# Performance work log

Measured on AMD Instinct MI355X. Metric: run time of the kernel, lower is better.

The kernel has to match this reference:

```python
import jax, jax.numpy as jnp
import numpy as np

PAD = 0  # pad_token_id sentinel used for word_starts and labels_arcs masking


def setup_inputs() -> dict:
    B, S, H, L = 16, 256, 768, 37
    key = jax.random.key(0)
    k1, k2, k3, k4, k5 = jax.random.split(key, 5)
    hidden = jax.random.normal(k1, (B, S, H), dtype=jnp.float32)
    # strictly-increasing subword start indices (1,3,5,...), zero-padded to S
    n_starts = S // 2
    row = jnp.concatenate([
        1 + 2 * jnp.arange(n_starts, dtype=jnp.int32),
        jnp.zeros(S - n_starts, dtype=jnp.int32),
    ])
    word_starts = jnp.tile(row[None, :], (B, 1))
    n_words = n_starts - 1  # spans are between consecutive starts
    la = jax.random.randint(k2, (B, S), 1, 2 * S, dtype=jnp.int32)
    labels_arcs = jnp.where(jnp.arange(S)[None, :] < n_words, la, PAD)
    labels_rels = jax.random.randint(k3, (B, S), 0, L, dtype=jnp.int32)
    W_arc = jax.random.normal(k4, (H + 1, H), dtype=jnp.float32) * 0.02
    W_rel = jax.random.normal(k5, (L, H + 1, H + 1), dtype=jnp.float32) * 0.02
    return dict(hidden=hidden, W_arc=W_arc, W_rel=W_rel,
                word_starts=word_starts, labels_arcs=labels_arcs,
                labels_rels=labels_rels)


def _merge_subword_tokens(hidden, word_starts):
    """Fused segment-mean: word j = mean(hidden[start_j:start_{j+1}])."""
    B, S, H = hidden.shape
    csum = jnp.concatenate(
        [jnp.zeros((B, 1, H), hidden.dtype), jnp.cumsum(hidden, axis=1)], axis=1)
    n_valid = jnp.sum(word_starts != PAD, axis=1)  # [B]
    start = word_starts  # [B,S]
    end = jnp.concatenate(
        [word_starts[:, 1:], jnp.zeros((B, 1), word_starts.dtype)], axis=1)
    valid = (jnp.arange(S)[None, :] + 1) < n_valid[:, None]  # word j needs start j+1
    s0 = jnp.take_along_axis(csum, start[..., None].astype(jnp.int32), axis=1)
    s1 = jnp.take_along_axis(csum, end[..., None].astype(jnp.int32), axis=1)
    length = jnp.clip(end - start, 1, None).astype(hidden.dtype)[..., None]
    return jnp.where(valid[..., None], (s1 - s0) / length, 0.0)  # [B,S,H]


def _with_ones(x):
    return jnp.concatenate([x, jnp.ones_like(x[..., :1])], axis=-1)


def reference(hidden, W_arc, W_rel, word_starts, labels_arcs, labels_rels):
    deps = _merge_subword_tokens(hidden, word_starts)            # [B,S,H]
    heads = jnp.concatenate([hidden, deps], axis=1)              # [B,2S,H]
    xa = _with_ones(deps)                                        # [B,S,H+1]
    arc_preds = jnp.einsum('bxi,ij,byj->bxy', xa, W_arc, heads)  # [B,S,2S]
    yr = _with_ones(heads)                                       # [B,2S,H+1]
    rel_preds = jnp.einsum('bxi,oij,byj->bxyo', xa, W_rel, yr)   # [B,S,2S,L]

    B, S, Y, L = rel_preds.shape
    mask = (labels_arcs != PAD).astype(hidden.dtype)             # [B,S]
    n = jnp.sum(mask)
    arc_lp = jax.nn.log_softmax(arc_preds, axis=-1)
    safe_arcs = jnp.clip(labels_arcs, 0, Y - 1)
    arc_ll = jnp.take_along_axis(arc_lp, safe_arcs[..., None], axis=-1)[..., 0]
    arc_loss = -jnp.sum(arc_ll * mask) / n

    idx = jnp.broadcast_to(safe_arcs[:, :, None, None], (B, S, 1, L))
    rel_sel = jnp.take_along_axis(rel_preds, idx, axis=2)[:, :, 0, :]  # [B,S,L]
    rel_lp = jax.nn.log_softmax(rel_sel, axis=-1)
    rel_ll = jnp.take_along_axis(rel_lp, labels_rels[..., None], axis=-1)[..., 0]
    rel_loss = -jnp.sum(rel_ll * mask) / n

    loss = arc_loss + rel_loss
    return loss, rel_preds, arc_preds
```

## Files before the change

### kernel.cpp

```cpp
#include <hip/hip_runtime.h>
#include <cmath>
#include <cstdint>


#define NB 16
#define SS 256
#define HH 768
#define LLn 37
#define YY 512

static const long long REL_ELEMS = (long long)NB * SS * YY * LLn;

typedef __bf16 bf16_t;
typedef __bf16 bf16x8 __attribute__((ext_vector_type(8)));
typedef float f32x4 __attribute__((ext_vector_type(4)));

__device__ __forceinline__ void async_copy16(const void* g, void* l) {
  __builtin_amdgcn_global_load_lds((__attribute__((address_space(1))) void*)(g),
                                   (__attribute__((address_space(3))) void*)(l),
                                   16, 0, 0);
}

__device__ __forceinline__ float wave_max(float v) {
  #pragma unroll
  for (int off = 32; off > 0; off >>= 1) v = fmaxf(v, __shfl_xor(v, off));
  return v;
}
__device__ __forceinline__ float wave_sum(float v) {
  #pragma unroll
  for (int off = 32; off > 0; off >>= 1) v += __shfl_xor(v, off);
  return v;
}


__global__ void hid_rows(const float* __restrict__ hidden, bf16_t* __restrict__ yrb) {
  const long long r = blockIdx.x;
  const int b = (int)(r >> 8), y = (int)(r & 255);
  const float4* src = (const float4*)(hidden + r * HH);
  bf16_t* dst = yrb + ((long long)b * YY + y) * HH;
  const int t = threadIdx.x;
  const float4 v = src[t];
  bf16_t o4[4] = {(bf16_t)v.x, (bf16_t)v.y, (bf16_t)v.z, (bf16_t)v.w};
  *(ushort4*)(dst + t * 4) = *(ushort4*)o4;
}

__global__ void build_deps2(const float* __restrict__ hidden,
                            const int* __restrict__ word_starts,
                            bf16_t* __restrict__ yrb) {
  const int x = blockIdx.x, b = blockIdx.y, t = threadIdx.x;
  const int ws0 = word_starts[b * SS + x];
  const int ws1 = (x + 1 < SS) ? word_starts[b * SS + x + 1] : 0;
  const bool valid = (x + 1 < SS) && (ws1 != 0);
  const int start = min(max(ws0, 0), SS);
  const int end = min(max(ws1, 0), SS);
  const int len = max(end - start, 1);
  const float inv = 1.0f / (float)len;
  const float* hb = hidden + (long long)b * SS * HH;
  bf16_t* yr = yrb + ((long long)b * YY + SS + x) * HH;
  for (int h = t; h < HH; h += 256) {
    float s = 0.f;
    if (valid) for (int tt = start; tt < end; ++tt) s += hb[(long long)tt * HH + h];
    yr[h] = (bf16_t)(valid ? s * inv : 0.f);
  }
}

__global__ void conv_warc(const float* __restrict__ W, bf16_t* __restrict__ Wab) {
  __shared__ float tbuf[32][33];
  const int i0 = blockIdx.x * 32, j0 = blockIdx.y * 32;
  const int tx = threadIdx.x, ty = threadIdx.y;
  for (int rr = 0; rr < 32; rr += 8)
    tbuf[ty + rr][tx] = W[(long long)(i0 + ty + rr) * HH + j0 + tx];
  __syncthreads();
  for (int rr = 0; rr < 32; rr += 8)
    Wab[(long long)(j0 + ty + rr) * HH + i0 + tx] = (bf16_t)tbuf[tx][ty + rr];
}

__global__ void conv_wrel(const float* __restrict__ W, bf16_t* __restrict__ Wb, int o0) {
  __shared__ float tbuf[32][33];
  const int o = o0 + blockIdx.z;
  const int i0 = blockIdx.x * 32, j0 = blockIdx.y * 32;
  const int tx = threadIdx.x, ty = threadIdx.y;
  const float* Wo = W + (long long)o * (HH + 1) * (HH + 1);
  for (int rr = 0; rr < 32; rr += 8)
    tbuf[ty + rr][tx] = Wo[(long long)(i0 + ty + rr) * (HH + 1) + j0 + tx];
  __syncthreads();
  bf16_t* Wbo = Wb + (long long)blockIdx.z * HH * HH;
  for (int rr = 0; rr < 32; rr += 8)
    Wbo[(long long)(j0 + ty + rr) * HH + i0 + tx] = (bf16_t)tbuf[tx][ty + rr];
}

__global__ void build_misc(const float* __restrict__ W_rel, const float* __restrict__ W_arc,
                           float* __restrict__ WbiasJ, bf16_t* __restrict__ Wb768,
                           float* __restrict__ bias768b, float* __restrict__ biasArc,
                           float* __restrict__ lossacc) {
  const int blk = blockIdx.x, t = threadIdx.x;
  if (blk < LLn) {
    const int o = blk;
    const float* Wo = W_rel + (long long)o * (HH + 1) * (HH + 1);
    for (int j = t; j < HH; j += 256)
      WbiasJ[(long long)o * HH + j] = Wo[(long long)HH * (HH + 1) + j];
    for (int i = t; i < HH; i += 256)
      Wb768[(long long)o * HH + i] = (bf16_t)Wo[(long long)i * (HH + 1) + HH];
    if (t == 0) bias768b[o] = Wo[(long long)HH * (HH + 1) + HH];
  } else {
    for (int j = t; j < HH; j += 256) biasArc[j] = W_arc[(long long)HH * HH + j];
    if (t == 0) { lossacc[0] = 0.f; lossacc[1] = 0.f; }
  }
}

__global__ void bias2_kernel(const bf16_t* __restrict__ yrb,
                             const bf16_t* __restrict__ Wb768,
                             const float* __restrict__ bias768b,
                             float* __restrict__ d_bias2) {
  const int r = blockIdx.x;
  const int b = r >> 8, x = r & 255;
  const bf16_t* dep = yrb + ((long long)b * YY + SS + x) * HH;
  const int w = threadIdx.x >> 6, lane = threadIdx.x & 63;
  __shared__ float drow[HH];
  for (int h = threadIdx.x; h < HH; h += 256) drow[h] = (float)dep[h];
  __syncthreads();
  for (int o = w; o < LLn; o += 4) {
    const bf16_t* wrow = Wb768 + (long long)o * HH;
    float s = 0.f;
    #pragma unroll
    for (int i = 0; i < HH / 64; i++) s += drow[lane + 64 * i] * (float)wrow[lane + 64 * i];
    s = wave_sum(s);
    if (lane == 0) d_bias2[(long long)r * 128 + o] = s + bias768b[o];
  }
}


template<int MODE>
__global__ __launch_bounds__(256)
void gemm_bt(const bf16_t* __restrict__ A, long long sAz, int lda, int aview,
             const bf16_t* __restrict__ B, long long sBz, int ldb,
             int K,
             float* __restrict__ Cf, bf16_t* __restrict__ Cb,
             long long sCz, int ldc,
             const float* __restrict__ cbias, int sbias,
             int OC, int o0, const float* __restrict__ bias_xo,
             int gy, int gx) {
  __shared__ __align__(16) char smem_raw[32768];
  bf16_t* const lds = (bf16_t*)smem_raw;
  const int tid = threadIdx.x;
  const int w = tid >> 6;
  const int lane = tid & 63;

  const int nwg = (int)gridDim.x;
  const int q = nwg >> 3, r8 = nwg & 7;
  const int xcd = (int)blockIdx.x & 7, sub = (int)blockIdx.x >> 3;
  const int lid = ((xcd < r8) ? xcd * (q + 1) : r8 * (q + 1) + (xcd - r8) * q) + sub;
  const int yb = lid % gy;
  const int t2g = lid / gy;
  const int xb = t2g % gx;
  const int z = t2g / gx;

  const long long row0 = (long long)yb * 128;
  const long long col0 = (long long)xb * 128;
  const bf16_t* Ab;
  if (aview) {
    const long long bb = row0 >> 8;
    Ab = A + (bb * 512 + 256 + (row0 & 255)) * (long long)lda;
  } else {
    Ab = A + z * sAz + row0 * lda;
  }
  const bf16_t* Bb = B + z * sBz + col0 * ldb;

  const int r_in = lane >> 2;
  const int kofs = (lane & 3) * 8;
  const bf16_t* gA0 = Ab + (long long)(w * 32 + r_in) * lda + kofs;
  const bf16_t* gA1 = gA0 + 16ll * lda;
  const bf16_t* gB0 = Bb + (long long)(w * 32 + r_in) * ldb + kofs;
  const bf16_t* gB1 = gB0 + 16ll * ldb;
  const int lA0 = (w * 32) * 32;
  const int lA1 = (w * 32 + 16) * 32;
  const int lB0 = 4096 + (w * 32) * 32;
  const int lB1 = 4096 + (w * 32 + 16) * 32;

  f32x4 acc[4][4];
  #pragma unroll
  for (int i = 0; i < 4; i++)
    #pragma unroll
    for (int j = 0; j < 4; j++)
      #pragma unroll
      for (int e = 0; e < 4; e++) acc[i][j][e] = 0.f;

  const int wm = (w >> 1) * 64, wn = (w & 1) * 64;
  const int fr = lane & 15;
  const int fq = lane >> 4;
  const int aoff = fq * 8;

  async_copy16(gA0, lds + lA0);
  async_copy16(gA1, lds + lA1);
  async_copy16(gB0, lds + lB0);
  async_copy16(gB1, lds + lB1);
  __syncthreads();

  int cur = 0;
  for (int k0 = 32; k0 < K; k0 += 32) {
    bf16_t* nb = lds + (cur ^ 1) * 8192;
    async_copy16(gA0 + k0, nb + lA0);
    async_copy16(gA1 + k0, nb + lA1);
    async_copy16(gB0 + k0, nb + lB0);
    async_copy16(gB1 + k0, nb + lB1);
    const bf16_t* cb = lds + cur * 8192;
    bf16x8 af[4], bfr[4];
    #pragma unroll
    for (int t = 0; t < 4; t++) af[t]  = *(const bf16x8*)&cb[(wm + t * 16 + fr) * 32 + aoff];
    #pragma unroll
    for (int t = 0; t < 4; t++) bfr[t] = *(const bf16x8*)&cb[4096 + (wn + t * 16 + fr) * 32 + aoff];
    #pragma unroll
    for (int tm = 0; tm < 4; tm++)
      #pragma unroll
      for (int tn = 0; tn < 4; tn++)
        acc[tm][tn] = __builtin_amdgcn_mfma_f32_16x16x32_bf16(af[tm], bfr[tn], acc[tm][tn], 0, 0, 0);
    __syncthreads();
    cur ^= 1;
  }
  {
    const bf16_t* cb = lds + cur * 8192;
    bf16x8 af[4], bfr[4];
    #pragma unroll
    for (int t = 0; t < 4; t++) af[t]  = *(const bf16x8*)&cb[(wm + t * 16 + fr) * 32 + aoff];
    #pragma unroll
    for (int t = 0; t < 4; t++) bfr[t] = *(const bf16x8*)&cb[4096 + (wn + t * 16 + fr) * 32 + aoff];
    #pragma unroll
    for (int tm = 0; tm < 4; tm++)
      #pragma unroll
      for (int tn = 0; tn < 4; tn++)
        acc[tm][tn] = __builtin_amdgcn_mfma_f32_16x16x32_bf16(af[tm], bfr[tn], acc[tm][tn], 0, 0, 0);
  }

  if (MODE == 2) {
    __syncthreads();
    float* ebuf = (float*)smem_raw;
    const int c = tid & 127;
    const int rgrp = tid >> 7;
    const int n = (int)col0 + c;
    const int x = n / OC;
    const int o = o0 + (n - x * OC);
    const float bias = bias_xo[(((long long)z << 8) + x) * 128 + o];
    float* outp = Cf + z * sCz + (long long)x * (YY * LLn) + o;
    #pragma unroll
    for (int ch = 0; ch < 4; ch++) {
      #pragma unroll
      for (int tn = 0; tn < 4; tn++)
        #pragma unroll
        for (int e = 0; e < 4; e++)
          ebuf[((w >> 1) * 16 + fq * 4 + e) * 132 + wn + tn * 16 + fr] = acc[ch][tn][e];
      __syncthreads();
      const long long ybase = row0 + (long long)rgrp * 64 + ch * 16;
      #pragma unroll
      for (int r = 0; r < 16; r++)
        outp[(ybase + r) * LLn] = ebuf[(rgrp * 16 + r) * 132 + c] + bias;
      __syncthreads();
    }
  } else {
    const int er = fq * 4;
    #pragma unroll
    for (int tn = 0; tn < 4; tn++) {
      const long long col = col0 + wn + tn * 16 + fr;
      const float bv = cbias ? cbias[(long long)z * sbias + col] : 0.f;
      #pragma unroll
      for (int tm = 0; tm < 4; tm++) {
        const int rl = wm + tm * 16 + er;
        if (MODE == 0) {
          bf16_t* dst = Cb + z * sCz + col;
          #pragma unroll
          for (int r = 0; r < 4; r++)
            dst[(row0 + rl + r) * (long long)ldc] = (bf16_t)(acc[tm][tn][r] + bv);
        } else {
          float* dst = Cf + z * sCz + col;
          #pragma unroll
          for (int r = 0; r < 4; r++)
            dst[(row0 + rl + r) * (long long)ldc] = acc[tm][tn][r] + bv;
        }
      }
    }
  }
}


__global__ void loss_kernel(const float* __restrict__ arc, const float* __restrict__ rel,
                            const int* __restrict__ la, const int* __restrict__ lr,
                            float* __restrict__ acc) {
  const int r = blockIdx.x;
  const int lane = threadIdx.x;
  const int lab = la[r];
  const float* ar = arc + (long long)r * YY;
  float v[8]; float m = -INFINITY;
  #pragma unroll
  for (int i = 0; i < 8; i++) { v[i] = ar[lane + 64 * i]; m = fmaxf(m, v[i]); }
  m = wave_max(m);
  float s = 0.f;
  #pragma unroll
  for (int i = 0; i < 8; i++) s += expf(v[i] - m);
  s = wave_sum(s);
  const float lse_a = m + logf(s);
  const int safe = lab < 0 ? 0 : (lab > YY - 1 ? YY - 1 : lab);
  const float* rr = rel + ((long long)r * YY + safe) * LLn;
  const float rv = (lane < LLn) ? rr[lane] : -INFINITY;
  const float m2 = wave_max(rv);
  const float s2 = wave_sum((lane < LLn) ? expf(rv - m2) : 0.f);
  const float lse_r = m2 + logf(s2);
  if (lane == 0 && lab != 0) {
    const float ll = (ar[safe] - lse_a) + (rr[lr[r]] - lse_r);
    atomicAdd(&acc[0], ll);
    atomicAdd(&acc[1], 1.f);
  }
}

__global__ void finalize(const float* __restrict__ acc, float* __restrict__ out) {
  out[0] = -acc[0] / acc[1];
}


extern "C" void kernel_launch(void* const* d_in, const int* in_sizes, int n_in,
                              void* d_out, int out_size, void* d_ws, size_t ws_size,
                              hipStream_t stream) {
  (void)in_sizes; (void)n_in; (void)out_size;
  const float* hidden      = (const float*)d_in[0];
  const float* W_arc       = (const float*)d_in[1];
  const float* W_rel       = (const float*)d_in[2];
  const int* word_starts   = (const int*)d_in[3];
  const int* labels_arcs   = (const int*)d_in[4];
  const int* labels_rels   = (const int*)d_in[5];

  float* out = (float*)d_out;
  float* rel_out = out + 1;
  float* arc_out = rel_out + REL_ELEMS;

  char* ws = (char*)d_ws;
  float* lossacc  = (float*)ws;
  bf16_t* yrb     = (bf16_t*)(ws + 256);
  bf16_t* Wab     = yrb + (size_t)NB * YY * HH;
  bf16_t* A1      = Wab + (size_t)HH * HH;
  bf16_t* Wb768   = A1 + (size_t)NB * SS * HH;
  float*  biasArc = (float*)(Wb768 + (size_t)128 * HH);
  float*  bias768b= biasArc + HH;
  float*  d_bias2 = bias768b + 128;
  float*  WbiasJ  = d_bias2 + (size_t)NB * SS * 128;
  bf16_t* Wbc     = (bf16_t*)(WbiasJ + (size_t)LLn * HH);

  const size_t fixedB = 256 +
      2 * ((size_t)NB * YY * HH + (size_t)HH * HH + (size_t)NB * SS * HH +
           (size_t)128 * HH) +
      4 * ((size_t)HH + 128 + (size_t)NB * SS * 128 + (size_t)LLn * HH);
  const size_t perOC = 2 * ((size_t)HH * HH + (size_t)NB * SS * HH);
  int OC = 1;
  if (ws_size > fixedB + perOC) {
    const size_t m = (ws_size - fixedB) / perOC;
    OC = (m > (size_t)LLn) ? LLn : (int)m;
  }
  bf16_t* M_p = Wbc + (size_t)OC * HH * HH;

  hid_rows<<<NB * SS, 192, 0, stream>>>(hidden, yrb);
  build_deps2<<<dim3(SS, NB), 256, 0, stream>>>(hidden, word_starts, yrb);
  conv_warc<<<dim3(24, 24), dim3(32, 8), 0, stream>>>(W_arc, Wab);
  build_misc<<<LLn + 1, 256, 0, stream>>>(W_rel, W_arc, WbiasJ, Wb768, bias768b, biasArc, lossacc);
  bias2_kernel<<<NB * SS, 256, 0, stream>>>(yrb, Wb768, bias768b, d_bias2);

  gemm_bt<0><<<192, 256, 0, stream>>>(
      yrb, 0, HH, 1, Wab, 0, HH, HH,
      nullptr, A1, 0, HH, biasArc, 0, 0, 0, nullptr, 32, 6);
  gemm_bt<1><<<128, 256, 0, stream>>>(
      A1, (long long)SS * HH, HH, 0,
      yrb, (long long)YY * HH, HH, HH,
      arc_out, nullptr, (long long)SS * YY, YY, nullptr, 0, 0, 0, nullptr, 2, 4);

  for (int o0 = 0; o0 < LLn; o0 += OC) {
    const int oc = (LLn - o0 < OC) ? (LLn - o0) : OC;
    conv_wrel<<<dim3(24, 24, oc), dim3(32, 8), 0, stream>>>(W_rel, Wbc, o0);
    gemm_bt<0><<<192 * oc, 256, 0, stream>>>(
        yrb, 0, HH, 1,
        Wbc, (long long)HH * HH, HH, HH,
        nullptr, M_p, HH, oc * HH, WbiasJ + (long long)o0 * HH, HH, 0, 0, nullptr, 32, 6);
    gemm_bt<2><<<128 * oc, 256, 0, stream>>>(
        yrb, (long long)YY * HH, HH, 0,
        M_p, (long long)SS * oc * HH, HH, HH,
        rel_out, nullptr, (long long)SS * YY * LLn, 0, nullptr, 0,
        oc, o0, d_bias2, 4, 2 * oc);
  }

  loss_kernel<<<NB * SS, 64, 0, stream>>>(arc_out, rel_out, labels_arcs, labels_rels, lossacc);
  finalize<<<1, 1, 0, stream>>>(lossacc, out);
}
```

Baseline: 962.1 us.

## Deepen GEMM LDS pipeline to four stages and use nontemporal output stores

Replaces the double-buffered K loop with a four-buffer pipeline. Three tiles are prefetched ahead, and explicit vmcnt waits with raw s_barrier calls take the place of __syncthreads. The K loop count is fixed at compile time (KST=24), and LDS per block doubles to 64KB, which may cut occupancy. All GEMM epilogue stores become nontemporal so the large rel/arc outputs are less likely to pollute the cache.

```diff
diff --git a/kernel.cpp b/kernel.cpp
--- a/kernel.cpp
+++ b/kernel.cpp
@@ -8,6 +8,7 @@
 #define HH 768
 #define LLn 37
 #define YY 512
+#define KST 24
 
 static const long long REL_ELEMS = (long long)NB * SS * YY * LLn;
 
@@ -134,13 +135,12 @@
 __global__ __launch_bounds__(256)
 void gemm_bt(const bf16_t* __restrict__ A, long long sAz, int lda, int aview,
              const bf16_t* __restrict__ B, long long sBz, int ldb,
-             int K,
              float* __restrict__ Cf, bf16_t* __restrict__ Cb,
              long long sCz, int ldc,
              const float* __restrict__ cbias, int sbias,
              int OC, int o0, const float* __restrict__ bias_xo,
              int gy, int gx) {
-  __shared__ __align__(16) char smem_raw[32768];
+  __shared__ __align__(16) char smem_raw[65536];
   bf16_t* const lds = (bf16_t*)smem_raw;
   const int tid = threadIdx.x;
   const int w = tid >> 6;
@@ -190,46 +190,51 @@
   const int fq = lane >> 4;
   const int aoff = fq * 8;
 
-  async_copy16(gA0, lds + lA0);
-  async_copy16(gA1, lds + lA1);
-  async_copy16(gB0, lds + lB0);
-  async_copy16(gB1, lds + lB1);
-  __syncthreads();
-
-  int cur = 0;
-  for (int k0 = 32; k0 < K; k0 += 32) {
-    bf16_t* nb = lds + (cur ^ 1) * 8192;
+  auto stage = [&](int t) {
+    bf16_t* nb = lds + (t & 3) * 8192;
+    const long long k0 = (long long)t * 32;
     async_copy16(gA0 + k0, nb + lA0);
     async_copy16(gA1 + k0, nb + lA1);
     async_copy16(gB0 + k0, nb + lB0);
     async_copy16(gB1 + k0, nb + lB1);
-    const bf16_t* cb = lds + cur * 8192;
+  };
+  auto compute_step = [&](const bf16_t* cb) {
     bf16x8 af[4], bfr[4];
     #pragma unroll
-    for (int t = 0; t < 4; t++) af[t]  = *(const bf16x8*)&cb[(wm + t * 16 + fr) * 32 + aoff];
-    #pragma unroll
-    for (int t = 0; t < 4; t++) bfr[t] = *(const bf16x8*)&cb[4096 + (wn + t * 16 + fr) * 32 + aoff];
+    for (int t4 = 0; t4 < 4; t4++) af[t4]  = *(const bf16x8*)&cb[(wm + t4 * 16 + fr) * 32 + aoff];
+    #pragma unroll
+    for (int t4 = 0; t4 < 4; t4++) bfr[t4] = *(const bf16x8*)&cb[4096 + (wn + t4 * 16 + fr) * 32 + aoff];
     #pragma unroll
     for (int tm = 0; tm < 4; tm++)
       #pragma unroll
       for (int tn = 0; tn < 4; tn++)
         acc[tm][tn] = __builtin_amdgcn_mfma_f32_16x16x32_bf16(af[tm], bfr[tn], acc[tm][tn], 0, 0, 0);
-    __syncthreads();
-    cur ^= 1;
-  }
-  {
-    const bf16_t* cb = lds + cur * 8192;
-    bf16x8 af[4], bfr[4];
-    #pragma unroll
-    for (int t = 0; t < 4; t++) af[t]  = *(const bf16x8*)&cb[(wm + t * 16 + fr) * 32 + aoff];
-    #pragma unroll
-    for (int t = 0; t < 4; t++) bfr[t] = *(const bf16x8*)&cb[4096 + (wn + t * 16 + fr) * 32 + aoff];
-    #pragma unroll
-    for (int tm = 0; tm < 4; tm++)
-      #pragma unroll
-      for (int tn = 0; tn < 4; tn++)
-        acc[tm][tn] = __builtin_amdgcn_mfma_f32_16x16x32_bf16(af[tm], bfr[tn], acc[tm][tn], 0, 0, 0);
-  }
+  };
+
+  stage(0); stage(1); stage(2);
+
+  #pragma unroll 1
+  for (int t = 0; t < KST - 3; ++t) {
+    stage(t + 3);
+    asm volatile("s_waitcnt vmcnt(12)" ::: "memory");
+    __builtin_amdgcn_s_barrier();
+    __builtin_amdgcn_sched_barrier(0);
+    compute_step(lds + (t & 3) * 8192);
+    __builtin_amdgcn_sched_barrier(0);
+    __builtin_amdgcn_s_barrier();
+  }
+  asm volatile("s_waitcnt vmcnt(8)" ::: "memory");
+  __builtin_amdgcn_s_barrier();
+  __builtin_amdgcn_sched_barrier(0);
+  compute_step(lds + ((KST - 3) & 3) * 8192);
+  asm volatile("s_waitcnt vmcnt(4)" ::: "memory");
+  __builtin_amdgcn_s_barrier();
+  __builtin_amdgcn_sched_barrier(0);
+  compute_step(lds + ((KST - 2) & 3) * 8192);
+  asm volatile("s_waitcnt vmcnt(0)" ::: "memory");
+  __builtin_amdgcn_s_barrier();
+  __builtin_amdgcn_sched_barrier(0);
+  compute_step(lds + ((KST - 1) & 3) * 8192);
 
   if (MODE == 2) {
     __syncthreads();
@@ -252,7 +257,8 @@
       const long long ybase = row0 + (long long)rgrp * 64 + ch * 16;
       #pragma unroll
       for (int r = 0; r < 16; r++)
-        outp[(ybase + r) * LLn] = ebuf[(rgrp * 16 + r) * 132 + c] + bias;
+        __builtin_nontemporal_store(ebuf[(rgrp * 16 + r) * 132 + c] + bias,
+                                    &outp[(ybase + r) * LLn]);
       __syncthreads();
     }
   } else {
@@ -268,12 +274,14 @@
           bf16_t* dst = Cb + z * sCz + col;
           #pragma unroll
           for (int r = 0; r < 4; r++)
-            dst[(row0 + rl + r) * (long long)ldc] = (bf16_t)(acc[tm][tn][r] + bv);
+            __builtin_nontemporal_store((bf16_t)(acc[tm][tn][r] + bv),
+                                        &dst[(row0 + rl + r) * (long long)ldc]);
         } else {
           float* dst = Cf + z * sCz + col;
           #pragma unroll
           for (int r = 0; r < 4; r++)
-            dst[(row0 + rl + r) * (long long)ldc] = acc[tm][tn][r] + bv;
+            __builtin_nontemporal_store(acc[tm][tn][r] + bv,
+                                        &dst[(row0 + rl + r) * (long long)ldc]);
         }
       }
     }
@@ -361,11 +369,11 @@
   bias2_kernel<<<NB * SS, 256, 0, stream>>>(yrb, Wb768, bias768b, d_bias2);
 
   gemm_bt<0><<<192, 256, 0, stream>>>(
-      yrb, 0, HH, 1, Wab, 0, HH, HH,
+      yrb, 0, HH, 1, Wab, 0, HH,
       nullptr, A1, 0, HH, biasArc, 0, 0, 0, nullptr, 32, 6);
   gemm_bt<1><<<128, 256, 0, stream>>>(
       A1, (long long)SS * HH, HH, 0,
-      yrb, (long long)YY * HH, HH, HH,
+      yrb, (long long)YY * HH, HH,
       arc_out, nullptr, (long long)SS * YY, YY, nullptr, 0, 0, 0, nullptr, 2, 4);
 
   for (int o0 = 0; o0 < LLn; o0 += OC) {
@@ -373,11 +381,11 @@
     conv_wrel<<<dim3(24, 24, oc), dim3(32, 8), 0, stream>>>(W_rel, Wbc, o0);
     gemm_bt<0><<<192 * oc, 256, 0, stream>>>(
         yrb, 0, HH, 1,
-        Wbc, (long long)HH * HH, HH, HH,
+        Wbc, (long long)HH * HH, HH,
         nullptr, M_p, HH, oc * HH, WbiasJ + (long long)o0 * HH, HH, 0, 0, nullptr, 32, 6);
     gemm_bt<2><<<128 * oc, 256, 0, stream>>>(
         yrb, (long long)YY * HH, HH, 0,
-        M_p, (long long)SS * oc * HH, HH, HH,
+        M_p, (long long)SS * oc * HH, HH,
         rel_out, nullptr, (long long)SS * YY * LLn, 0, nullptr, 0,
         oc, o0, d_bias2, 4, 2 * oc);
   }
```

New measurement: 1.102 ms. 1.15x slower.
